# Performance work log

Hardware: AMD Instinct MI355X
Metric: run time of the kernel (lower is better)

Reference implementation:

```python
import jax, jax.numpy as jnp
import numpy as np
import math

MU = 5; ETA = 1.0; ITERS = 3
SIGMA_C = 1.0; SIGMA_S = 1.6 * SIGMA_C
SIGMA_M = 3.0; RHO = 0.99; TAU = 0.7
MAX_T = int(math.floor(3 * SIGMA_C))  # 3
MAX_S = int(math.floor(3 * SIGMA_M))  # 9
DELTA = 1.0
B, C, X, Y = 4, 1, 512, 512


def _gpdf(v, sig):
    return math.exp(-v * v / (2.0 * sig * sig)) / (math.sqrt(2.0 * math.pi) * sig)


def _sobel(img):
    k = jnp.array([[-1., -2., -1.], [0., 0., 0.], [1., 2., 1.]], dtype=img.dtype)
    kern = jnp.stack([k, k.T])[:, None]  # [2,1,3,3] OIHW
    return jax.lax.conv_general_dilated(img, kern, (1, 1), [(1, 1), (1, 1)],
                                        dimension_numbers=('NCHW', 'OIHW', 'NCHW'))


def _gather_flat(arr, idx):
    # arr [b,c,x,y], idx int [b,x,y] flattened spatial index (px*Y+py)
    b, c, x, y = arr.shape
    flat = arr.reshape(b, c, x * y)
    idxb = jnp.broadcast_to(idx.reshape(b, 1, x * y), (b, c, x * y))
    return jnp.take_along_axis(flat, idxb, axis=2).reshape(b, c, x, y)


def _safe_norm(v):
    m = jnp.linalg.norm(v, axis=1, keepdims=True)
    return v / jnp.where(m == 0, 1.0, m)


def _etf(images):
    b, c, x, y = images.shape
    sob = _sobel(images)                                   # [b,2,x,y]
    mag = jnp.linalg.norm(sob, axis=1, keepdims=True)      # [b,1,x,y]
    mag = mag / jnp.max(mag)
    mag_p = jnp.pad(mag, ((0, 0), (0, 0), (MU, MU), (MU, MU)))
    sobel_X = mag[:, None]                                 # [b,1,1,x,y]
    tang = _safe_norm(jnp.stack([-sob[:, 1], sob[:, 0]], axis=1))
    K = 2 * MU + 1
    for _ in range(ITERS):
        for ori in ('V', 'H'):
            tang_p = jnp.pad(tang, ((0, 0), (0, 0), (MU, MU), (MU, MU)))
            tang_X = tang[:, None]                         # [b,1,2,x,y]
            if ori == 'V':
                tang_Y = jnp.stack([tang_p[:, :, i:i + x, MU:MU + y] for i in range(K)], axis=1)
                sobel_Y = jnp.stack([mag_p[:, :, i:i + x, MU:MU + y] for i in range(K)], axis=1)
            else:
                tang_Y = jnp.stack([tang_p[:, :, MU:MU + x, i:i + y] for i in range(K)], axis=1)
                sobel_Y = jnp.stack([mag_p[:, :, MU:MU + x, i:i + y] for i in range(K)], axis=1)
            # weight: magnitude term * direction term / 2
            w = (jnp.tanh(ETA * (sobel_Y - sobel_X)) + 1.0) \
                * jnp.sum(tang_X * tang_Y, axis=2, keepdims=True) * 0.5
            tang = _safe_norm(jnp.sum(tang_Y * w, axis=1))
    return tang


def _dog(images, etf):
    b, c, x, y = images.shape
    xi, yi = jnp.meshgrid(jnp.arange(x, dtype=images.dtype),
                          jnp.arange(y, dtype=images.dtype), indexing='ij')
    idx0 = jnp.broadcast_to(jnp.stack([xi, yi])[None], (b, 2, x, y))
    per = jnp.stack([-etf[:, 1], etf[:, 0]], axis=1)       # perpendicular to flow
    dog = jnp.zeros_like(images)
    tw = 0.0
    for t in range(-MAX_T, MAX_T + 1):
        pts = idx0 + DELTA * per * t
        px = jnp.round(jnp.clip(pts[:, 0], 0, x - 1)).astype(jnp.int32)
        py = jnp.round(jnp.clip(pts[:, 1], 0, y - 1)).astype(jnp.int32)
        il = _gather_flat(images, px * y + py)
        gw = _gpdf(t, SIGMA_C) - RHO * _gpdf(t, SIGMA_S)
        tw += gw
        dog = dog + il * gw
    return dog / tw


def _fdog_float(images):
    b, c, x, y = images.shape
    etf = _etf(images)
    dog = _dog(images, etf)
    fdog = jnp.zeros_like(images)
    tw = 0.0
    xi, yi = jnp.meshgrid(jnp.arange(x, dtype=jnp.int32),
                          jnp.arange(y, dtype=jnp.int32), indexing='ij')
    for s_dir in (-1, 1):
        px = jnp.broadcast_to(xi[None], (b, x, y))
        py = jnp.broadcast_to(yi[None], (b, x, y))
        for s in range(0 if s_dir == 1 else 1, MAX_S + 1):
            if s != 0:
                p_etf = _gather_flat(etf, px * y + py)     # flow at current points
                fx = px.astype(images.dtype) + DELTA * p_etf[:, 0] * s_dir
                fy = py.astype(images.dtype) + DELTA * p_etf[:, 1] * s_dir
                px = jnp.round(jnp.clip(fx, 0, x - 1)).astype(jnp.int32)
                py = jnp.round(jnp.clip(fy, 0, y - 1)).astype(jnp.int32)
            f_s = _gather_flat(dog, px * y + py)
            gw = _gpdf(s, SIGMA_M)
            tw += gw
            fdog = fdog + f_s * gw
    return fdog / tw


def setup_inputs() -> dict:
    key = jax.random.key(0)
    images = jax.random.uniform(key, (B, C, X, Y), dtype=jnp.float32)
    return {"images": images}


def reference(images):
    fdog = _fdog_float(images)
    edges = ~((fdog < 0) & (1.0 + jnp.tanh(fdog) < TAU))
    return edges.astype(jnp.int32)
```

## Files before the change

kernel.cpp:

```cpp
#include <hip/hip_runtime.h>
#include <math.h>

#pragma clang fp contract(off)

#define BN 4
#define SX 512
#define SY 512
#define NPIX (BN * SX * SY)
#define MU 5
#define MB (1024 * 1024)
#define NBLOCKS 4096

struct DogW  { float g[7];  float tw; };
struct FdogW { float g[10]; float tw; };

__device__ __forceinline__ float fast_tanh_f32(float dF) {
    double d = (double)dF;
    double y = fabs(d);
    double t = expm1(2.0 * y);
    double r = t / (t + 2.0);
    if (y > 350.0) r = 1.0;
    return (float)copysign(r, d);
}

__device__ __forceinline__ float img_at(const float* __restrict__ img, int b, int x, int y) {
    if (x < 0 || x >= SX || y < 0 || y >= SY) return 0.0f;
    return img[(size_t)b * SX * SY + (size_t)x * SY + y];
}

__global__ void k_sobel(const float* __restrict__ img, float* __restrict__ mag,
                        float2* __restrict__ tang, float* __restrict__ partial) {
#pragma clang fp contract(off)
    int yi = blockIdx.x * blockDim.x + threadIdx.x;
    int xi = blockIdx.y;
    int b  = blockIdx.z;

    float v00 = img_at(img, b, xi - 1, yi - 1);
    float v01 = img_at(img, b, xi - 1, yi    );
    float v02 = img_at(img, b, xi - 1, yi + 1);
    float v10 = img_at(img, b, xi,     yi - 1);
    float v12 = img_at(img, b, xi,     yi + 1);
    float v20 = img_at(img, b, xi + 1, yi - 1);
    float v21 = img_at(img, b, xi + 1, yi    );
    float v22 = img_at(img, b, xi + 1, yi + 1);

    float s0 = (-1.0f * v00);
    s0 = s0 + (-2.0f * v01);
    s0 = s0 + (-1.0f * v02);
    s0 = s0 + ( 1.0f * v20);
    s0 = s0 + ( 2.0f * v21);
    s0 = s0 + ( 1.0f * v22);
    float s1 = (-1.0f * v00);
    s1 = s1 + ( 1.0f * v02);
    s1 = s1 + (-2.0f * v10);
    s1 = s1 + ( 2.0f * v12);
    s1 = s1 + (-1.0f * v20);
    s1 = s1 + ( 1.0f * v22);

    float m = sqrtf((s0 * s0) + (s1 * s1));
    size_t idx = (size_t)b * SX * SY + (size_t)xi * SY + yi;
    mag[idx] = m;

    float tx = -s1, ty = s0;
    float n = sqrtf((tx * tx) + (ty * ty));
    float d = (n == 0.0f) ? 1.0f : n;
    tang[idx] = make_float2(tx / d, ty / d);

    float wm = m;
    for (int off = 32; off > 0; off >>= 1) wm = fmaxf(wm, __shfl_down(wm, off, 64));
    __shared__ float red[4];
    int lane = threadIdx.x & 63;
    int wid  = threadIdx.x >> 6;
    if (lane == 0) red[wid] = wm;
    __syncthreads();
    if (threadIdx.x == 0) {
        float bm = fmaxf(fmaxf(red[0], red[1]), fmaxf(red[2], red[3]));
        int bid = blockIdx.x + gridDim.x * (blockIdx.y + gridDim.y * blockIdx.z);
        partial[bid] = bm;
    }
}

__global__ void k_reduce(const float* __restrict__ partial, unsigned int* __restrict__ maxbits) {
    float m = 0.0f;
    for (int i = threadIdx.x; i < NBLOCKS; i += 256) m = fmaxf(m, partial[i]);
    for (int off = 32; off > 0; off >>= 1) m = fmaxf(m, __shfl_down(m, off, 64));
    __shared__ float red[4];
    int lane = threadIdx.x & 63;
    int wid  = threadIdx.x >> 6;
    if (lane == 0) red[wid] = m;
    __syncthreads();
    if (threadIdx.x == 0) {
        float bm = fmaxf(fmaxf(red[0], red[1]), fmaxf(red[2], red[3]));
        *maxbits = __float_as_uint(bm);
    }
}

__global__ void k_norm(float* __restrict__ mag, const unsigned int* __restrict__ maxbits) {
    int i = blockIdx.x * blockDim.x + threadIdx.x;
    float mx = __uint_as_float(*maxbits);
    mag[i] = mag[i] / mx;
}

__global__ void k_tanh(const float* __restrict__ mag, const unsigned int* __restrict__ maxbits,
                       float* __restrict__ TV, float* __restrict__ TH) {
#pragma clang fp contract(off)
    int yi = blockIdx.x * blockDim.x + threadIdx.x;
    int xi = blockIdx.y;
    int b  = blockIdx.z;
    size_t base = (size_t)b * SX * SY;
    size_t idx  = base + (size_t)xi * SY + yi;
    float mx = __uint_as_float(*maxbits);
    float cm = mag[idx] / mx;
#pragma unroll
    for (int k = 1; k <= 5; ++k) {
        if (xi + k < SX) {
            float nm = mag[idx + (size_t)k * SY] / mx;
            TV[(size_t)(k - 1) * NPIX + idx] = fast_tanh_f32(nm - cm);
        }
    }
#pragma unroll
    for (int k = 1; k <= 5; ++k) {
        if (yi + k < SY) {
            float nm = mag[idx + k] / mx;
            TH[(size_t)(k - 1) * NPIX + idx] = fast_tanh_f32(nm - cm);
        }
    }
}

#define VTY 32
#define VTX 16
__global__ __launch_bounds__(256) void k_etf_v(const float2* __restrict__ tsrc,
                                               float2* __restrict__ tdst,
                                               const float* __restrict__ TV) {
#pragma clang fp contract(off)
    int ty  = threadIdx.x & 31;
    int txw = threadIdx.x >> 5;
    int y0 = blockIdx.x * VTY;
    int x0 = blockIdx.y * VTX;
    int b  = blockIdx.z;
    size_t base = (size_t)b * SX * SY;

    __shared__ __align__(16) float2 sT[VTX + 2 * MU][VTY];
    __shared__ __align__(16) float  sTV[5][VTX + MU][VTY];

    int tid = threadIdx.x;
    for (int i = tid; i < (VTX + 2 * MU) * (VTY / 4) * 2; i += 256) {
        int r = i >> 4;
        int c = i & 15;
        int gx = x0 - MU + r;
        if (gx >= 0 && gx < SX)
            ((float4*)&sT[r][0])[c] = ((const float4*)(tsrc + base + (size_t)gx * SY + y0))[c];
    }
    for (int i = tid; i < 5 * (VTX + MU) * (VTY / 4); i += 256) {
        int j   = i / ((VTX + MU) * (VTY / 4));
        int rem = i - j * ((VTX + MU) * (VTY / 4));
        int r   = rem >> 3;
        int c   = rem & 7;
        int gx  = x0 - MU + r;
        if (gx >= 0 && gx < SX)
            ((float4*)&sTV[j][r][0])[c] =
                ((const float4*)(TV + (size_t)j * NPIX + base + (size_t)gx * SY + y0))[c];
    }
    __syncthreads();

    int yi = y0 + ty;
#pragma unroll
    for (int sub = 0; sub < 2; ++sub) {
        int tx = txw + (sub << 3);
        int xi = x0 + tx;
        size_t idx = base + (size_t)xi * SY + yi;

        float2 ct = sT[tx + MU][ty];
        float sx = 0.0f, sy = 0.0f;
#pragma unroll
        for (int k = -MU; k <= MU; ++k) {
            int nx = xi + k;
            if (nx < 0 || nx >= SX) continue;
            float2 nt = sT[tx + MU + k][ty];
            float th;
            if (k > 0)      th =  sTV[k - 1][tx + MU][ty];
            else if (k < 0) th = -sTV[-k - 1][tx + MU + k][ty];
            else            th =  0.0f;
            float dot = (ct.x * nt.x) + (ct.y * nt.y);
            float w   = ((th + 1.0f) * dot) * 0.5f;
            sx = sx + (nt.x * w);
            sy = sy + (nt.y * w);
        }
        float n = sqrtf((sx * sx) + (sy * sy));
        float d = (n == 0.0f) ? 1.0f : n;
        tdst[idx] = make_float2(sx / d, sy / d);
    }
}

__global__ __launch_bounds__(256) void k_etf_h(const float2* __restrict__ tsrc,
                                               float2* __restrict__ tdst,
                                               const float* __restrict__ TH,
                                               const float* __restrict__ img,
                                               float* __restrict__ dogout,
                                               DogW dw, int do_dog) {
#pragma clang fp contract(off)
    int tid = threadIdx.x;
    int xi  = blockIdx.y;
    int b   = blockIdx.z;
    size_t base    = (size_t)b * SX * SY;
    size_t rowbase = base + (size_t)xi * SY;

    __shared__ __align__(16) float2 sT[SY];
    __shared__ __align__(16) float  sTH[5][SY];

    ((float4*)sT)[tid] = ((const float4*)(tsrc + rowbase))[tid];
    for (int i = tid; i < 5 * (SY / 4); i += 256) {
        int j = i >> 7;
        int c = i & 127;
        ((float4*)&sTH[0][0])[i] = ((const float4*)(TH + (size_t)j * NPIX + rowbase))[c];
    }
    __syncthreads();

#pragma unroll
    for (int half = 0; half < 2; ++half) {
        int yi = tid + half * 256;
        float2 ct = sT[yi];
        float sx = 0.0f, sy = 0.0f;
#pragma unroll
        for (int k = -MU; k <= MU; ++k) {
            int ny = yi + k;
            if (ny < 0 || ny >= SY) continue;
            float2 nt = sT[ny];
            float th;
            if (k > 0)      th =  sTH[k - 1][yi];
            else if (k < 0) th = -sTH[-k - 1][ny];
            else            th =  0.0f;
            float dot = (ct.x * nt.x) + (ct.y * nt.y);
            float w   = ((th + 1.0f) * dot) * 0.5f;
            sx = sx + (nt.x * w);
            sy = sy + (nt.y * w);
        }
        float n = sqrtf((sx * sx) + (sy * sy));
        float d = (n == 0.0f) ? 1.0f : n;
        float ex = sx / d;
        float ey = sy / d;
        tdst[rowbase + yi] = make_float2(ex, ey);

        if (do_dog) {
            float perx = -ey;
            float pery =  ex;
            float xf = (float)xi, yf = (float)yi;
            float acc = 0.0f;
#pragma unroll
            for (int t = -3; t <= 3; ++t) {
                float tf  = (float)t;
                float ptx = xf + (perx * tf);
                float pty = yf + (pery * tf);
                int px = (int)rintf(fminf(fmaxf(ptx, 0.0f), (float)(SX - 1)));
                int py = (int)rintf(fminf(fmaxf(pty, 0.0f), (float)(SY - 1)));
                float il = img[base + (size_t)px * SY + py];
                acc = acc + (il * dw.g[t + 3]);
            }
            dogout[rowbase + yi] = acc / dw.tw;
        }
    }
}

__global__ void k_etf(const float2* __restrict__ tsrc, float2* __restrict__ tdst,
                      const float* __restrict__ mag, int vert) {
#pragma clang fp contract(off)
    int yi = blockIdx.x * blockDim.x + threadIdx.x;
    int xi = blockIdx.y;
    int b  = blockIdx.z;
    size_t base = (size_t)b * SX * SY;
    size_t idx  = base + (size_t)xi * SY + yi;

    float  cm = mag[idx];
    float2 ct = tsrc[idx];

    float sx = 0.0f, sy = 0.0f;
    for (int k = -MU; k <= MU; ++k) {
        int nx = xi + (vert ? k : 0);
        int ny = yi + (vert ? 0 : k);
        if (nx < 0 || nx >= SX || ny < 0 || ny >= SY) continue;
        size_t nidx = base + (size_t)nx * SY + ny;
        float  nm = mag[nidx];
        float2 nt = tsrc[nidx];
        float dot = (ct.x * nt.x) + (ct.y * nt.y);
        float th  = (float)tanh((double)(nm - cm));
        float w   = ((th + 1.0f) * dot) * 0.5f;
        sx = sx + (nt.x * w);
        sy = sy + (nt.y * w);
    }
    float n = sqrtf((sx * sx) + (sy * sy));
    float d = (n == 0.0f) ? 1.0f : n;
    tdst[idx] = make_float2(sx / d, sy / d);
}

__global__ void k_dog(const float* __restrict__ img, const float2* __restrict__ etf,
                      float* __restrict__ dog, DogW w) {
#pragma clang fp contract(off)
    int yi = blockIdx.x * blockDim.x + threadIdx.x;
    int xi = blockIdx.y;
    int b  = blockIdx.z;
    size_t base = (size_t)b * SX * SY;
    size_t idx  = base + (size_t)xi * SY + yi;

    float2 e = etf[idx];
    float perx = -e.y;
    float pery =  e.x;
    float xf = (float)xi, yf = (float)yi;

    float acc = 0.0f;
#pragma unroll
    for (int t = -3; t <= 3; ++t) {
        float tf  = (float)t;
        float ptx = xf + (perx * tf);
        float pty = yf + (pery * tf);
        int px = (int)rintf(fminf(fmaxf(ptx, 0.0f), (float)(SX - 1)));
        int py = (int)rintf(fminf(fmaxf(pty, 0.0f), (float)(SY - 1)));
        float il = img[base + (size_t)px * SY + py];
        acc = acc + (il * w.g[t + 3]);
    }
    dog[idx] = acc / w.tw;
}

__global__ void k_fdog(const float* __restrict__ dog, const float2* __restrict__ etf,
                       int* __restrict__ out, FdogW w) {
#pragma clang fp contract(off)
    int yi = blockIdx.x * blockDim.x + threadIdx.x;
    int xi = blockIdx.y;
    int b  = blockIdx.z;
    size_t base = (size_t)b * SX * SY;
    size_t idx  = base + (size_t)xi * SY + yi;

    float d1[9];
    float d2[10];
    float2 e0 = etf[idx];
    float2 e1 = e0, e2 = e0;
    int p1x = xi, p1y = yi;
    int p2x = xi, p2y = yi;
    d2[0] = dog[idx];

#pragma unroll
    for (int s = 1; s <= 9; ++s) {
        float fx1 = (float)p1x + (e1.x * -1.0f);
        float fy1 = (float)p1y + (e1.y * -1.0f);
        p1x = (int)rintf(fminf(fmaxf(fx1, 0.0f), (float)(SX - 1)));
        p1y = (int)rintf(fminf(fmaxf(fy1, 0.0f), (float)(SY - 1)));
        size_t i1 = base + (size_t)p1x * SY + p1y;
        float fx2 = (float)p2x + (e2.x * 1.0f);
        float fy2 = (float)p2y + (e2.y * 1.0f);
        p2x = (int)rintf(fminf(fmaxf(fx2, 0.0f), (float)(SX - 1)));
        p2y = (int)rintf(fminf(fmaxf(fy2, 0.0f), (float)(SY - 1)));
        size_t i2 = base + (size_t)p2x * SY + p2y;

        d1[s - 1] = dog[i1];
        d2[s]     = dog[i2];
        if (s < 9) {
            e1 = etf[i1];
            e2 = etf[i2];
        }
    }

    float acc = 0.0f;
#pragma unroll
    for (int s = 1; s <= 9; ++s) acc = acc + (d1[s - 1] * w.g[s]);
    acc = acc + (d2[0] * w.g[0]);
#pragma unroll
    for (int s = 1; s <= 9; ++s) acc = acc + (d2[s] * w.g[s]);

    float fv = acc / w.tw;
    float th = 1.0f + fast_tanh_f32(fv);
    out[idx] = ((fv < 0.0f) && (th < 0.7f)) ? 0 : 1;
}

static double gpdf(double v, double sig) {
    return exp(-(v * v) / (2.0 * sig * sig)) / (sqrt(2.0 * M_PI) * sig);
}

extern "C" void kernel_launch(void* const* d_in, const int* in_sizes, int n_in,
                              void* d_out, int out_size, void* d_ws, size_t ws_size,
                              hipStream_t stream) {
    const float* img = (const float*)d_in[0];
    int* out = (int*)d_out;
    char* ws = (char*)d_ws;

    const size_t need = (size_t)60 * MB + NBLOCKS * sizeof(float) + 4;
    bool fast = ws_size >= need;

    float*  mag = (float*)(ws);
    float2* tA  = (float2*)(ws + (size_t)4  * MB);
    float2* tB  = (float2*)(ws + (size_t)12 * MB);
    float*  TV  = (float*)(ws + (size_t)20 * MB);
    float*  TH  = (float*)(ws + (size_t)40 * MB);
    size_t  tail = fast ? (size_t)60 * MB : (size_t)20 * MB;
    float*        partial = (float*)(ws + tail);
    unsigned int* maxbits = (unsigned int*)(ws + tail + NBLOCKS * sizeof(float));

    dim3 blk(256, 1, 1);
    dim3 grd(SY / 256, SX, BN);
    dim3 vgrd(SY / VTY, SX / VTX, BN);
    dim3 hgrd(1, SX, BN);

    DogW dw;
    {
        double tw = 0.0;
        for (int t = -3; t <= 3; ++t) {
            double g = gpdf((double)t, 1.0) - 0.99 * gpdf((double)t, 1.6);
            dw.g[t + 3] = (float)g;
            tw += g;
        }
        dw.tw = (float)tw;
    }
    FdogW fw;
    {
        for (int s = 0; s <= 9; ++s) fw.g[s] = (float)gpdf((double)s, 3.0);
        double tw = 0.0;
        for (int s = 1; s <= 9; ++s) tw += gpdf((double)s, 3.0);
        for (int s = 0; s <= 9; ++s) tw += gpdf((double)s, 3.0);
        fw.tw = (float)tw;
    }

    k_sobel<<<grd, blk, 0, stream>>>(img, mag, tA, partial);
    k_reduce<<<1, 256, 0, stream>>>(partial, maxbits);

    float2* src = tA;
    float2* dst = tB;
    if (fast) {
        float* dogbuf = mag;
        k_tanh<<<grd, blk, 0, stream>>>(mag, maxbits, TV, TH);
        for (int it = 0; it < 3; ++it) {
            k_etf_v<<<vgrd, blk, 0, stream>>>(src, dst, TV);
            { float2* t = src; src = dst; dst = t; }
            k_etf_h<<<hgrd, blk, 0, stream>>>(src, dst, TH, img, dogbuf, dw, it == 2);
            { float2* t = src; src = dst; dst = t; }
        }
        k_fdog<<<grd, blk, 0, stream>>>(dogbuf, src, out, fw);
    } else {
        k_norm<<<NPIX / 256, 256, 0, stream>>>(mag, maxbits);
        for (int it = 0; it < 3; ++it) {
            k_etf<<<grd, blk, 0, stream>>>(src, dst, mag, 1);
            { float2* t = src; src = dst; dst = t; }
            k_etf<<<grd, blk, 0, stream>>>(src, dst, mag, 0);
            { float2* t = src; src = dst; dst = t; }
        }
        float* dogbuf = (src == tA) ? (float*)tB : (float*)tA;
        k_dog<<<grd, blk, 0, stream>>>(img, src, dogbuf, dw);
        k_fdog<<<grd, blk, 0, stream>>>(dogbuf, src, out, fw);
    }
}
```

Before: 193.3 us.

## Fuse vertical and horizontal ETF passes into one tiled kernel with halo recompute

Merges the separate vertical and horizontal edge-tangent-flow smoothing kernels into a single kernel working on 4x64 tiles. The vertical result for a tile plus a horizontal halo is computed into shared memory, and the horizontal pass then reads it from there. This removes one launch per iteration and the global write and re-read of the intermediate tangent field. In exchange it recomputes the halo columns and uses a larger shared-memory footprint per block.

```diff
diff --git a/kernel.cpp b/kernel.cpp
--- a/kernel.cpp
+++ b/kernel.cpp
@@ -127,59 +127,77 @@
     }
 }
 
-#define VTY 32
-#define VTX 16
-__global__ __launch_bounds__(256) void k_etf_v(const float2* __restrict__ tsrc,
-                                               float2* __restrict__ tdst,
-                                               const float* __restrict__ TV) {
-#pragma clang fp contract(off)
-    int ty  = threadIdx.x & 31;
-    int txw = threadIdx.x >> 5;
-    int y0 = blockIdx.x * VTY;
-    int x0 = blockIdx.y * VTX;
+#define FTX 4
+#define FTY 64
+#define ETY (FTY + 2 * MU)
+#define SCOL (FTY + 16)
+__global__ __launch_bounds__(256) void k_etf_vh(const float2* __restrict__ tsrc,
+                                                float2* __restrict__ tdst,
+                                                const float* __restrict__ TV,
+                                                const float* __restrict__ TH,
+                                                const float* __restrict__ img,
+                                                float* __restrict__ dogout,
+                                                DogW dw, int do_dog) {
+#pragma clang fp contract(off)
+    int tid = threadIdx.x;
+    int y0 = blockIdx.x * FTY;
+    int x0 = blockIdx.y * FTX;
     int b  = blockIdx.z;
     size_t base = (size_t)b * SX * SY;
 
-    __shared__ __align__(16) float2 sT[VTX + 2 * MU][VTY];
-    __shared__ __align__(16) float  sTV[5][VTX + MU][VTY];
-
-    int tid = threadIdx.x;
-    for (int i = tid; i < (VTX + 2 * MU) * (VTY / 4) * 2; i += 256) {
-        int r = i >> 4;
-        int c = i & 15;
+    __shared__ __align__(16) float2 sT[FTX + 2 * MU][SCOL];
+    __shared__ __align__(16) float  sTV[5][FTX + MU][SCOL];
+    __shared__ __align__(16) float2 sV[FTX][SCOL];
+    __shared__ __align__(16) float  sTH[5][FTX][FTY + 8];
+
+    for (int i = tid; i < (FTX + 2 * MU) * (SCOL / 2); i += 256) {
+        int r  = i / (SCOL / 2);
+        int c  = i % (SCOL / 2);
         int gx = x0 - MU + r;
-        if (gx >= 0 && gx < SX)
-            ((float4*)&sT[r][0])[c] = ((const float4*)(tsrc + base + (size_t)gx * SY + y0))[c];
-    }
-    for (int i = tid; i < 5 * (VTX + MU) * (VTY / 4); i += 256) {
-        int j   = i / ((VTX + MU) * (VTY / 4));
-        int rem = i - j * ((VTX + MU) * (VTY / 4));
-        int r   = rem >> 3;
-        int c   = rem & 7;
+        int gy = y0 - 8 + 2 * c;
+        if (gx >= 0 && gx < SX && gy >= 0 && gy < SY)
+            ((float4*)&sT[r][0])[c] =
+                *((const float4*)(tsrc + base + (size_t)gx * SY + gy));
+    }
+    for (int i = tid; i < 5 * (FTX + MU) * (SCOL / 4); i += 256) {
+        int j   = i / ((FTX + MU) * (SCOL / 4));
+        int rem = i - j * ((FTX + MU) * (SCOL / 4));
+        int r   = rem / (SCOL / 4);
+        int c   = rem % (SCOL / 4);
         int gx  = x0 - MU + r;
-        if (gx >= 0 && gx < SX)
+        int gy  = y0 - 8 + 4 * c;
+        if (gx >= 0 && gx < SX && gy >= 0 && gy < SY)
             ((float4*)&sTV[j][r][0])[c] =
-                ((const float4*)(TV + (size_t)j * NPIX + base + (size_t)gx * SY + y0))[c];
+                *((const float4*)(TV + (size_t)j * NPIX + base + (size_t)gx * SY + gy));
+    }
+    for (int i = tid; i < 5 * FTX * ((FTY + 8) / 4); i += 256) {
+        int j   = i / (FTX * ((FTY + 8) / 4));
+        int rem = i - j * (FTX * ((FTY + 8) / 4));
+        int r   = rem / ((FTY + 8) / 4);
+        int c   = rem % ((FTY + 8) / 4);
+        int gx  = x0 + r;
+        int gy  = y0 - 8 + 4 * c;
+        if (gy >= 0)
+            ((float4*)&sTH[j][r][0])[c] =
+                *((const float4*)(TH + (size_t)j * NPIX + base + (size_t)gx * SY + gy));
     }
     __syncthreads();
 
-    int yi = y0 + ty;
-#pragma unroll
-    for (int sub = 0; sub < 2; ++sub) {
-        int tx = txw + (sub << 3);
-        int xi = x0 + tx;
-        size_t idx = base + (size_t)xi * SY + yi;
-
-        float2 ct = sT[tx + MU][ty];
+    for (int p = tid; p < FTX * ETY; p += 256) {
+        int r  = p / ETY;
+        int e  = p % ETY;
+        int xi = x0 + r;
+        int c  = e + 3;
+        float2 ct = sT[r + MU][c];
         float sx = 0.0f, sy = 0.0f;
 #pragma unroll
         for (int k = -MU; k <= MU; ++k) {
             int nx = xi + k;
             if (nx < 0 || nx >= SX) continue;
-            float2 nt = sT[tx + MU + k][ty];
+            float2 nt = sT[r + MU + k][c];
             float th;
-            if (k > 0)      th =  sTV[k - 1][tx + MU][ty];
-            else if (k < 0) th = -sTV[-k - 1][tx + MU + k][ty];
+            if (k > 0)      th =  sTV[k - 1][r + MU][c];
+            else if (k < 0) th = -sTV[-k - 1][r + MU + k][c];
             else            th =  0.0f;
             float dot = (ct.x * nt.x) + (ct.y * nt.y);
             float w   = ((th + 1.0f) * dot) * 0.5f;
@@ -188,47 +206,27 @@
         }
         float n = sqrtf((sx * sx) + (sy * sy));
         float d = (n == 0.0f) ? 1.0f : n;
-        tdst[idx] = make_float2(sx / d, sy / d);
-    }
-}
-
-__global__ __launch_bounds__(256) void k_etf_h(const float2* __restrict__ tsrc,
-                                               float2* __restrict__ tdst,
-                                               const float* __restrict__ TH,
-                                               const float* __restrict__ img,
-                                               float* __restrict__ dogout,
-                                               DogW dw, int do_dog) {
-#pragma clang fp contract(off)
-    int tid = threadIdx.x;
-    int xi  = blockIdx.y;
-    int b   = blockIdx.z;
-    size_t base    = (size_t)b * SX * SY;
-    size_t rowbase = base + (size_t)xi * SY;
-
-    __shared__ __align__(16) float2 sT[SY];
-    __shared__ __align__(16) float  sTH[5][SY];
-
-    ((float4*)sT)[tid] = ((const float4*)(tsrc + rowbase))[tid];
-    for (int i = tid; i < 5 * (SY / 4); i += 256) {
-        int j = i >> 7;
-        int c = i & 127;
-        ((float4*)&sTH[0][0])[i] = ((const float4*)(TH + (size_t)j * NPIX + rowbase))[c];
+        sV[r][c] = make_float2(sx / d, sy / d);
     }
     __syncthreads();
 
-#pragma unroll
-    for (int half = 0; half < 2; ++half) {
-        int yi = tid + half * 256;
-        float2 ct = sT[yi];
+    {
+        int r  = tid >> 6;
+        int yl = tid & 63;
+        int xi = x0 + r;
+        int yi = y0 + yl;
+        size_t rowbase = base + (size_t)xi * SY;
+
+        float2 ct = sV[r][yl + 8];
         float sx = 0.0f, sy = 0.0f;
 #pragma unroll
         for (int k = -MU; k <= MU; ++k) {
             int ny = yi + k;
             if (ny < 0 || ny >= SY) continue;
-            float2 nt = sT[ny];
+            float2 nt = sV[r][yl + 8 + k];
             float th;
-            if (k > 0)      th =  sTH[k - 1][yi];
-            else if (k < 0) th = -sTH[-k - 1][ny];
+            if (k > 0)      th =  sTH[k - 1][r][yl + 8];
+            else if (k < 0) th = -sTH[-k - 1][r][yl + 8 + k];
             else            th =  0.0f;
             float dot = (ct.x * nt.x) + (ct.y * nt.y);
             float w   = ((th + 1.0f) * dot) * 0.5f;
@@ -395,8 +393,7 @@
 
     dim3 blk(256, 1, 1);
     dim3 grd(SY / 256, SX, BN);
-    dim3 vgrd(SY / VTY, SX / VTX, BN);
-    dim3 hgrd(1, SX, BN);
+    dim3 vhgrd(SY / FTY, SX / FTX, BN);
 
     DogW dw;
     {
@@ -426,9 +423,7 @@
         float* dogbuf = mag;
         k_tanh<<<grd, blk, 0, stream>>>(mag, maxbits, TV, TH);
         for (int it = 0; it < 3; ++it) {
-            k_etf_v<<<vgrd, blk, 0, stream>>>(src, dst, TV);
-            { float2* t = src; src = dst; dst = t; }
-            k_etf_h<<<hgrd, blk, 0, stream>>>(src, dst, TH, img, dogbuf, dw, it == 2);
+            k_etf_vh<<<vhgrd, blk, 0, stream>>>(src, dst, TV, TH, img, dogbuf, dw, it == 2);
             { float2* t = src; src = dst; dst = t; }
         }
         k_fdog<<<grd, blk, 0, stream>>>(dogbuf, src, out, fw);
```

Measured after the change: 213.4 us. 10.4% more time.
